# Kernel optimization log

Measured on AMD Instinct MI355X. Metric: run time of the kernel, lower is better.

Reference implementation:

```python
import jax, jax.numpy as jnp
import numpy as np

V = 32000; D = 256; H = 8; L = 2; FF = 1024; S = 512; B = 32
M = 4096          # mem_max_entries
NC = 10           # num_classes
K = 4             # retrieve top-k
TH = 0.5          # write threshold
EPS = 1e-8


def setup_inputs() -> dict:
    key = jax.random.key(0)
    ks = jax.random.split(key, 24)
    s = 0.02
    def nrm(k, shape):
        return jax.random.normal(k, shape, jnp.float32) * s
    return {
        "input_ids": jax.random.randint(ks[0], (B, S), 0, V),
        "tok_emb": nrm(ks[1], (V, D)),
        "pos_emb": nrm(ks[2], (S, D)),
        # per-layer params stacked on leading dim L
        "Wqkv": nrm(ks[3], (L, 3 * D, D)), "bqkv": jnp.zeros((L, 3 * D)),
        "Wo": nrm(ks[4], (L, D, D)), "bo": jnp.zeros((L, D)),
        "ln1_g": jnp.ones((L, D)), "ln1_b": jnp.zeros((L, D)),
        "W1": nrm(ks[5], (L, FF, D)), "b1": jnp.zeros((L, FF)),
        "W2": nrm(ks[6], (L, D, FF)), "b2": jnp.zeros((L, D)),
        "ln2_g": jnp.ones((L, D)), "ln2_b": jnp.zeros((L, D)),
        # write gate MLP (d -> d -> 1, sigmoid)
        "Wg1": nrm(ks[7], (D, D)), "bg1": jnp.zeros((D,)),
        "Wg2": nrm(ks[8], (1, D)), "bg2": jnp.zeros((1,)),
        # classifier
        "Wc": nrm(ks[9], (NC, D)), "bc": jnp.zeros((NC,)),
    }


def _layer_norm(x, g, b):
    m = x.mean(-1, keepdims=True)
    v = ((x - m) ** 2).mean(-1, keepdims=True)
    return (x - m) / jnp.sqrt(v + 1e-5) * g + b


def _encoder_layer(x, Wqkv, bqkv, Wo, bo, g1, b1, W1, bf1, W2, bf2, g2, b2):
    # post-LN TransformerEncoderLayer, relu activation, batch_first
    Bx, Sx, Dx = x.shape
    dh = Dx // H
    qkv = x @ Wqkv.T + bqkv                     # [B,S,3D]
    q, k, v = jnp.split(qkv, 3, axis=-1)
    def heads(t):
        return t.reshape(Bx, Sx, H, dh).transpose(0, 2, 1, 3)  # [B,H,S,dh]
    q, k, v = heads(q), heads(k), heads(v)
    scores = jnp.einsum("bhqd,bhkd->bhqk", q, k) / jnp.sqrt(jnp.float32(dh))
    attn = jax.nn.softmax(scores, axis=-1)
    o = jnp.einsum("bhqk,bhkd->bhqd", attn, v)
    o = o.transpose(0, 2, 1, 3).reshape(Bx, Sx, Dx)
    o = o @ Wo.T + bo
    x = _layer_norm(x + o, g1, b1)
    ff = jax.nn.relu(x @ W1.T + bf1) @ W2.T + bf2
    return _layer_norm(x + ff, g2, b2)


def reference(input_ids, tok_emb, pos_emb, Wqkv, bqkv, Wo, bo, ln1_g, ln1_b,
              W1, b1, W2, b2, ln2_g, ln2_b, Wg1, bg1, Wg2, bg2, Wc, bc):
    Bx, Sx = input_ids.shape
    x = tok_emb[input_ids] + pos_emb[jnp.arange(Sx)][None, :, :]
    for l in range(L):
        x = _encoder_layer(x, Wqkv[l], bqkv[l], Wo[l], bo[l], ln1_g[l], ln1_b[l],
                           W1[l], b1[l], W2[l], b2[l], ln2_g[l], ln2_b[l])
    h = x                                        # [B,S,D]
    cls_state = h[:, 0, :]                       # [B,D]

    # --- write gate: per-token store into external memory (capped FIFO scatter) ---
    flat_h = h.reshape(-1, D)                    # [B*S, D]
    probs = jax.nn.sigmoid(jax.nn.relu(flat_h @ Wg1.T + bg1) @ Wg2.T + bg2)[:, 0]
    mask = probs > TH                            # [B*S]
    slot = jnp.cumsum(mask.astype(jnp.int32)) - 1
    valid = mask & (slot < M)
    idx = jnp.where(valid, slot, M)              # overflow -> dummy row M
    mem = jnp.zeros((M + 1, D), jnp.float32).at[idx].set(flat_h)[:M]
    count = jnp.minimum(mask.sum(), M)
    occupied = jnp.arange(M) < count             # [M]

    # --- top-k cosine retrieval with CLS as query ---
    qn = cls_state / (jnp.linalg.norm(cls_state, axis=-1, keepdims=True) + EPS)
    kn = mem / (jnp.linalg.norm(mem, axis=-1, keepdims=True) + EPS)
    sims = qn @ kn.T                             # [B,M]
    sims = jnp.where(occupied[None, :], sims, -1e9)
    top_sims, top_idx = jax.lax.top_k(sims, K)   # [B,K]
    vals = mem[top_idx]                          # [B,K,D] (unoccupied rows are zero)
    attn = jax.nn.softmax(top_sims, axis=-1)
    mem_vec = jnp.einsum("bk,bkd->bd", attn, vals)
    mem_vec = jnp.where(count > 0, mem_vec, 0.0)

    cls_aug = cls_state + mem_vec
    return cls_aug @ Wc.T + bc                   # [B,NC]
```

## Files before the change

kernel.cpp:

```cpp
#include <hip/hip_runtime.h>
#include <math.h>

#define D_   256
#define H_   8
#define L_   2
#define FF_  1024
#define S_   512
#define B_   32
#define M_   4096
#define NC_  10
#define ROWS (B_*S_)

typedef __attribute__((ext_vector_type(8))) short bf16x8;
typedef __attribute__((ext_vector_type(4))) float f32x4;

__device__ __forceinline__ float wave_sum(float v) {
#pragma unroll
  for (int off = 1; off < 64; off <<= 1) v += __shfl_xor(v, off, 64);
  return v;
}

__device__ __forceinline__ unsigned short bf16_rne(float x) {
  unsigned int b = __float_as_uint(x);
  return (unsigned short)((b + 0x7FFFu + ((b >> 16) & 1u)) >> 16);
}
__device__ __forceinline__ float bf16_f(unsigned short h) {
  return __uint_as_float(((unsigned int)h) << 16);
}
__device__ __forceinline__ unsigned int cvt_pk_bf16(float a, float b) {
  unsigned int r;
  asm volatile("v_cvt_pk_bf16_f32 %0, %1, %2" : "=v"(r) : "v"(a), "v"(b));
  return r;
}

__device__ __forceinline__ void cvt_store(unsigned short* Hq, unsigned short* Lq,
                                          int off, float4 v) {
  float f[4] = {v.x, v.y, v.z, v.w};
  unsigned short h[4], l[4];
#pragma unroll
  for (int i = 0; i < 4; i++) {
    h[i] = bf16_rne(f[i]);
    l[i] = bf16_rne(f[i] - bf16_f(h[i]));
  }
  uint2 hp, lp;
  hp.x = (unsigned int)h[0] | ((unsigned int)h[1] << 16);
  hp.y = (unsigned int)h[2] | ((unsigned int)h[3] << 16);
  lp.x = (unsigned int)l[0] | ((unsigned int)l[1] << 16);
  lp.y = (unsigned int)l[2] | ((unsigned int)l[3] << 16);
  *(uint2*)&Hq[off] = hp;
  *(uint2*)&Lq[off] = lp;
}

__device__ __forceinline__ bf16x8 ld_frag(const unsigned short* p, int off) {
  union { uint2 u[2]; bf16x8 v; } x;
  x.u[0] = *(const uint2*)(p + off);
  x.u[1] = *(const uint2*)(p + off + 4);
  return x.v;
}

__global__ __launch_bounds__(256) void emb_kernel(const int* __restrict__ ids,
                                                  const float* __restrict__ tok,
                                                  const float* __restrict__ pos,
                                                  float* __restrict__ x) {
  const int row  = blockIdx.x * 4 + (threadIdx.x >> 6);
  const int lane = threadIdx.x & 63;
  const int id = ids[row];
  const int s  = row & (S_ - 1);
  const float4 t = *(const float4*)(tok + (size_t)id * D_ + lane * 4);
  const float4 p = *(const float4*)(pos + (size_t)s  * D_ + lane * 4);
  float4 r; r.x = t.x + p.x; r.y = t.y + p.y; r.z = t.z + p.z; r.w = t.w + p.w;
  *(float4*)(x + (size_t)row * D_ + lane * 4) = r;
}

#define LP 36
template<int BM, int RELU>
__global__ __launch_bounds__(512, 4) void gemm_mfma(const float* __restrict__ A,
                                                    const float* __restrict__ Bm,
                                                    const float* __restrict__ bias,
                                                    float* __restrict__ C,
                                                    int M, int N, int K) {
  constexpr int WGM = BM / 64;
  constexpr int WGN = 8 / WGM;
  constexpr int WN  = 128 / WGN;
  constexpr int FN  = WN / 16;
  __shared__ __align__(16) unsigned short Ah[BM * LP];
  __shared__ __align__(16) unsigned short Al[BM * LP];
  __shared__ __align__(16) unsigned short Bh[128 * LP];
  __shared__ __align__(16) unsigned short Bl[128 * LP];

  const int tid  = threadIdx.x;
  const int lane = tid & 63;
  const int wid  = tid >> 6;
  const int wm = wid / WGN, wn = wid % WGN;
  const int m0 = blockIdx.y * BM, n0 = blockIdx.x * 128;
  const int lrow  = lane & 15;
  const int khalf = (lane >> 4) * 8;

  const int srow = tid >> 3;
  const int kq   = (tid & 7) << 2;
  const float* Aptr = A + (size_t)(m0 + srow) * K + kq;
  const float* Bptr = Bm + (size_t)(n0 + srow) * K + kq;

  f32x4 acc[4][FN];
#pragma unroll
  for (int i = 0; i < 4; i++)
#pragma unroll
    for (int j = 0; j < FN; j++) acc[i][j] = (f32x4){0.f, 0.f, 0.f, 0.f};

  float4 pa[BM / 64], pb[2];
#pragma unroll
  for (int j = 0; j < BM / 64; j++) pa[j] = *(const float4*)(Aptr + (size_t)j * 64 * K);
#pragma unroll
  for (int j = 0; j < 2; j++) pb[j] = *(const float4*)(Bptr + (size_t)j * 64 * K);

  for (int k0 = 0; k0 < K; k0 += 32) {
    const int kn = (k0 + 32 < K) ? (k0 + 32) : k0;
    float4 na[BM / 64], nb[2];
#pragma unroll
    for (int j = 0; j < BM / 64; j++) na[j] = *(const float4*)(Aptr + (size_t)j * 64 * K + kn);
#pragma unroll
    for (int j = 0; j < 2; j++) nb[j] = *(const float4*)(Bptr + (size_t)j * 64 * K + kn);

    __syncthreads();
#pragma unroll
    for (int j = 0; j < BM / 64; j++)
      cvt_store(Ah, Al, (srow + j * 64) * LP + kq, pa[j]);
#pragma unroll
    for (int j = 0; j < 2; j++)
      cvt_store(Bh, Bl, (srow + j * 64) * LP + kq, pb[j]);
    __syncthreads();

    bf16x8 ah[4], al[4], bh[FN], bl[FN];
#pragma unroll
    for (int fm = 0; fm < 4; fm++) {
      const int r = (wm * 64 + fm * 16 + lrow) * LP + khalf;
      ah[fm] = ld_frag(Ah, r);
      al[fm] = ld_frag(Al, r);
    }
#pragma unroll
    for (int fn = 0; fn < FN; fn++) {
      const int r = (wn * WN + fn * 16 + lrow) * LP + khalf;
      bh[fn] = ld_frag(Bh, r);
      bl[fn] = ld_frag(Bl, r);
    }
#pragma unroll
    for (int fm = 0; fm < 4; fm++)
#pragma unroll
      for (int fn = 0; fn < FN; fn++) {
        acc[fm][fn] = __builtin_amdgcn_mfma_f32_16x16x32_bf16(ah[fm], bh[fn], acc[fm][fn], 0, 0, 0);
        acc[fm][fn] = __builtin_amdgcn_mfma_f32_16x16x32_bf16(ah[fm], bl[fn], acc[fm][fn], 0, 0, 0);
        acc[fm][fn] = __builtin_amdgcn_mfma_f32_16x16x32_bf16(al[fm], bh[fn], acc[fm][fn], 0, 0, 0);
      }
#pragma unroll
    for (int j = 0; j < BM / 64; j++) pa[j] = na[j];
#pragma unroll
    for (int j = 0; j < 2; j++) pb[j] = nb[j];
  }

#pragma unroll
  for (int fm = 0; fm < 4; fm++)
#pragma unroll
    for (int fn = 0; fn < FN; fn++) {
      const int mrow = m0 + wm * 64 + fm * 16 + (lane >> 4) * 4;
      const int ncol = n0 + wn * WN + fn * 16 + (lane & 15);
      const float bi = bias[ncol];
#pragma unroll
      for (int r = 0; r < 4; r++) {
        float v = acc[fm][fn][r] + bi;
        if (RELU) v = fmaxf(v, 0.f);
        C[(size_t)(mrow + r) * N + ncol] = v;
      }
    }
}

#define KP 36
#define VP 516
__global__ __launch_bounds__(1024, 4) void attn_mfma(const float* __restrict__ qkv,
                                                     float* __restrict__ o) {
  __shared__ __align__(16) unsigned short Kh[512 * KP];
  __shared__ __align__(16) unsigned short Kl[512 * KP];
  __shared__ __align__(16) unsigned short Vth[32 * VP];
  __shared__ __align__(16) unsigned short Vtl[32 * VP];

  const int bh = blockIdx.x;
  const int b = bh >> 3, h = bh & 7;
  const int tid = threadIdx.x;
  const int lane = tid & 63;
  const int wv = tid >> 6;
  const float* base = qkv + (size_t)b * (S_ * 768) + h * 32;

  if (tid < 512) {
    const int slot = tid;
    const int s5 = slot & 31;
    const int orig = (slot & ~31) + 8 * ((s5 >> 2) & 3) + ((s5 >> 4) << 2) + (s5 & 3);
    const float* p = base + (size_t)orig * 768 + 256;
#pragma unroll
    for (int j = 0; j < 8; j++) {
      const float4 v = *(const float4*)(p + j * 4);
      cvt_store(Kh, Kl, slot * KP + j * 4, v);
    }
  } else {
    const int u  = tid - 512;
    const int kp = u & 255;
    const int dg = (u >> 8) * 16;
    const float* p0 = base + (size_t)(2 * kp) * 768 + 512 + dg;
    const float* p1 = p0 + 768;
    float v0[16], v1[16];
#pragma unroll
    for (int i = 0; i < 4; i++) {
      *(float4*)&v0[i * 4] = *(const float4*)(p0 + i * 4);
      *(float4*)&v1[i * 4] = *(const float4*)(p1 + i * 4);
    }
#pragma unroll
    for (int d = 0; d < 16; d++) {
      const unsigned short h0 = bf16_rne(v0[d]), h1 = bf16_rne(v1[d]);
      const unsigned short l0 = bf16_rne(v0[d] - bf16_f(h0));
      const unsigned short l1 = bf16_rne(v1[d] - bf16_f(h1));
      *(unsigned int*)&Vth[(dg + d) * VP + 2 * kp] = (unsigned int)h0 | ((unsigned int)h1 << 16);
      *(unsigned int*)&Vtl[(dg + d) * VP + 2 * kp] = (unsigned int)l0 | ((unsigned int)l1 << 16);
    }
  }

  const int q0 = wv * 32;
  bf16x8 qh[2], ql[2];
#pragma unroll
  for (int f = 0; f < 2; f++) {
    const float* qp = base + (size_t)(q0 + f * 16 + (lane & 15)) * 768 + ((lane >> 4) * 8);
    float qq[8];
    *(float4*)&qq[0] = *(const float4*)qp;
    *(float4*)&qq[4] = *(const float4*)(qp + 4);
    bf16x8 vh, vl;
#pragma unroll
    for (int j = 0; j < 8; j++) {
      const float sv = qq[j] * 0.17677669529663687f;
      const unsigned short hh = bf16_rne(sv);
      vh[j] = (short)hh;
      vl[j] = (short)bf16_rne(sv - bf16_f(hh));
    }
    qh[f] = vh; ql[f] = vl;
  }

  __syncthreads();

  f32x4 oacc[2][2];
#pragma unroll
  for (int i = 0; i < 2; i++)
#pragma unroll
    for (int j = 0; j < 2; j++) oacc[i][j] = (f32x4){0.f, 0.f, 0.f, 0.f};
  float lacc[2] = {0.f, 0.f};

  for (int kt = 0; kt < S_; kt += 32) {
    bf16x8 kah[2], kal[2];
#pragma unroll
    for (int u = 0; u < 2; u++) {
      const int off = (kt + u * 16 + (lane & 15)) * KP + ((lane >> 4) * 8);
      kah[u] = ld_frag(Kh, off);
      kal[u] = ld_frag(Kl, off);
    }
    bf16x8 vah[2], val[2];
#pragma unroll
    for (int df = 0; df < 2; df++) {
      const int off = (df * 16 + (lane & 15)) * VP + kt + ((lane >> 4) * 8);
      vah[df] = ld_frag(Vth, off);
      val[df] = ld_frag(Vtl, off);
    }
    f32x4 s[2][2];
#pragma unroll
    for (int u = 0; u < 2; u++)
#pragma unroll
      for (int f = 0; f < 2; f++) {
        f32x4 a = (f32x4){0.f, 0.f, 0.f, 0.f};
        a = __builtin_amdgcn_mfma_f32_16x16x32_bf16(kal[u], qh[f], a, 0, 0, 0);
        a = __builtin_amdgcn_mfma_f32_16x16x32_bf16(kah[u], ql[f], a, 0, 0, 0);
        a = __builtin_amdgcn_mfma_f32_16x16x32_bf16(kah[u], qh[f], a, 0, 0, 0);
        s[u][f] = a;
      }
#pragma unroll
    for (int f = 0; f < 2; f++) {
      union { unsigned int w[4]; bf16x8 v; } ph, pl;
#pragma unroll
      for (int u = 0; u < 2; u++) {
        const float p0 = __expf(s[u][f][0]);
        const float p1 = __expf(s[u][f][1]);
        const float p2 = __expf(s[u][f][2]);
        const float p3 = __expf(s[u][f][3]);
        lacc[f] += (p0 + p1) + (p2 + p3);
        const unsigned int h01 = cvt_pk_bf16(p0, p1);
        const unsigned int h23 = cvt_pk_bf16(p2, p3);
        const float r0 = p0 - __uint_as_float(h01 << 16);
        const float r1 = p1 - __uint_as_float(h01 & 0xffff0000u);
        const float r2 = p2 - __uint_as_float(h23 << 16);
        const float r3 = p3 - __uint_as_float(h23 & 0xffff0000u);
        ph.w[u * 2 + 0] = h01;
        ph.w[u * 2 + 1] = h23;
        pl.w[u * 2 + 0] = cvt_pk_bf16(r0, r1);
        pl.w[u * 2 + 1] = cvt_pk_bf16(r2, r3);
      }
#pragma unroll
      for (int df = 0; df < 2; df++) {
        oacc[df][f] = __builtin_amdgcn_mfma_f32_16x16x32_bf16(val[df], ph.v, oacc[df][f], 0, 0, 0);
        oacc[df][f] = __builtin_amdgcn_mfma_f32_16x16x32_bf16(vah[df], pl.v, oacc[df][f], 0, 0, 0);
        oacc[df][f] = __builtin_amdgcn_mfma_f32_16x16x32_bf16(vah[df], ph.v, oacc[df][f], 0, 0, 0);
      }
    }
  }

#pragma unroll
  for (int f = 0; f < 2; f++) {
    lacc[f] += __shfl_xor(lacc[f], 16, 64);
    lacc[f] += __shfl_xor(lacc[f], 32, 64);
  }
#pragma unroll
  for (int f = 0; f < 2; f++) {
    const float inv = 1.f / lacc[f];
    const int q = q0 + f * 16 + (lane & 15);
    float* op = o + (size_t)(b * S_ + q) * D_ + h * 32;
#pragma unroll
    for (int df = 0; df < 2; df++) {
      const int dbase = df * 16 + (lane >> 4) * 4;
#pragma unroll
      for (int r = 0; r < 4; r++)
        op[dbase + r] = oacc[df][f][r] * inv;
    }
  }
}

__global__ __launch_bounds__(256) void add_ln(const float* __restrict__ x,
                                              const float* __restrict__ y,
                                              const float* __restrict__ g,
                                              const float* __restrict__ bta,
                                              float* __restrict__ out) {
  const int row  = blockIdx.x * 4 + (threadIdx.x >> 6);
  const int lane = threadIdx.x & 63;
  const size_t base = (size_t)row * D_ + lane * 4;
  const float4 xv = *(const float4*)(x + base);
  const float4 yv = *(const float4*)(y + base);
  float v[4] = {xv.x + yv.x, xv.y + yv.y, xv.z + yv.z, xv.w + yv.w};
  float s = v[0] + v[1] + v[2] + v[3];
  s = wave_sum(s);
  const float mean = s * (1.f / 256.f);
  float d[4] = {v[0] - mean, v[1] - mean, v[2] - mean, v[3] - mean};
  float sq = d[0] * d[0] + d[1] * d[1] + d[2] * d[2] + d[3] * d[3];
  sq = wave_sum(sq);
  const float inv = 1.f / sqrtf(sq * (1.f / 256.f) + 1e-5f);
  const float4 gv = *(const float4*)(g + lane * 4);
  const float4 bv = *(const float4*)(bta + lane * 4);
  float4 r;
  r.x = d[0] * inv * gv.x + bv.x; r.y = d[1] * inv * gv.y + bv.y;
  r.z = d[2] * inv * gv.z + bv.z; r.w = d[3] * inv * gv.w + bv.w;
  *(float4*)(out + base) = r;
}

__global__ __launch_bounds__(256) void gate_mask(const float* __restrict__ t,
                                                 const float* __restrict__ Wg2,
                                                 const float* __restrict__ bg2,
                                                 int* __restrict__ mask) {
  const int row  = blockIdx.x * 4 + (threadIdx.x >> 6);
  const int lane = threadIdx.x & 63;
  const float4 tv = *(const float4*)(t + (size_t)row * D_ + lane * 4);
  const float4 wv = *(const float4*)(Wg2 + lane * 4);
  float s = tv.x * wv.x + tv.y * wv.y + tv.z * wv.z + tv.w * wv.w;
  s = wave_sum(s);
  if (lane == 0) mask[row] = (s + bg2[0]) > 0.f ? 1 : 0;
}

__global__ __launch_bounds__(256) void scan_kernel(const int* __restrict__ mask,
                                                   int* __restrict__ slots,
                                                   int* __restrict__ countp) {
  __shared__ int wtot[4];
  const int tid = threadIdx.x;
  const int lane = tid & 63, wid = tid >> 6;
  const int base = tid * 64;
  int s = 0;
#pragma unroll 8
  for (int i = 0; i < 64; i++) s += mask[base + i];
  int inc = s;
#pragma unroll
  for (int off = 1; off < 64; off <<= 1) {
    const int t = __shfl_up(inc, off, 64);
    if (lane >= off) inc += t;
  }
  if (lane == 63) wtot[wid] = inc;
  __syncthreads();
  int woff = 0;
#pragma unroll
  for (int w = 0; w < 4; w++) woff += (w < wid) ? wtot[w] : 0;
  const int total = wtot[0] + wtot[1] + wtot[2] + wtot[3];
  if (tid == 0) countp[0] = total < M_ ? total : M_;
  int run = woff + inc - s;
  for (int i = 0; i < 64; i++) {
    const int r = base + i;
    const int mk = mask[r];
    slots[r] = (mk && run < M_) ? run : -1;
    run += mk;
  }
}

__global__ __launch_bounds__(256) void scatter_kernel(const float* __restrict__ h,
                                                      const int* __restrict__ slots,
                                                      float* __restrict__ mem) {
  const int row  = blockIdx.x * 4 + (threadIdx.x >> 6);
  const int lane = threadIdx.x & 63;
  const int sl = slots[row];
  if (sl >= 0)
    *(float4*)(mem + (size_t)sl * D_ + lane * 4) =
        *(const float4*)(h + (size_t)row * D_ + lane * 4);
}

__global__ __launch_bounds__(256) void qnorm_kernel(const float* __restrict__ h,
                                                    float* __restrict__ qden) {
  const int b    = blockIdx.x * 4 + (threadIdx.x >> 6);
  const int lane = threadIdx.x & 63;
  const float4 c = *(const float4*)(h + (size_t)b * S_ * D_ + lane * 4);
  float sq = c.x * c.x + c.y * c.y + c.z * c.z + c.w * c.w;
  sq = wave_sum(sq);
  if (lane == 0) qden[b] = sqrtf(sq) + 1e-8f;
}

__global__ __launch_bounds__(256) void sims_kernel(const float* __restrict__ h,
                                                   const float* __restrict__ mem,
                                                   const float* __restrict__ qden,
                                                   const int* __restrict__ countp,
                                                   float* __restrict__ sims) {
  __shared__ float cls[B_ * D_];
  __shared__ float qd[B_];
  const int tid = threadIdx.x;
  const int lane = tid & 63, wid = tid >> 6;
  for (int i = tid; i < B_ * D_ / 4; i += 256) {
    const int flat = i * 4;
    const int b = flat >> 8, d = flat & 255;
    *(float4*)&cls[flat] = *(const float4*)(h + (size_t)b * S_ * D_ + d);
  }
  if (tid < B_) qd[tid] = qden[tid];
  __syncthreads();
  const int count = countp[0];
  const int r = blockIdx.x * 4 + wid;
  const float4 m4 = *(const float4*)(mem + (size_t)r * D_ + lane * 4);
  float sq = m4.x * m4.x + m4.y * m4.y + m4.z * m4.z + m4.w * m4.w;
  sq = wave_sum(sq);
  const float rn = sqrtf(sq) + 1e-8f;
  if (r < count) {
    for (int b = 0; b < B_; b++) {
      const float4 c4 = *(const float4*)&cls[b * D_ + lane * 4];
      float dt = m4.x * c4.x + m4.y * c4.y + m4.z * c4.z + m4.w * c4.w;
      dt = wave_sum(dt);
      if (lane == 0) sims[b * M_ + r] = dt / (qd[b] * rn);
    }
  } else if (lane == 0) {
    for (int b = 0; b < B_; b++) sims[b * M_ + r] = -1e9f;
  }
}

__global__ __launch_bounds__(256) void topk_mix(const float* __restrict__ h,
                                                const float* __restrict__ mem,
                                                const float* __restrict__ simsg,
                                                const int* __restrict__ countp,
                                                const float* __restrict__ Wc,
                                                const float* __restrict__ bc,
                                                float* __restrict__ out) {
  __shared__ float sims[M_];
  __shared__ float cls[D_];
  __shared__ float wv4[4];
  __shared__ int   wi4[4];
  __shared__ float aug[D_];
  __shared__ float tv[4];
  __shared__ int   tix[4];

  const int b = blockIdx.x, tid = threadIdx.x;
  const int lane = tid & 63, wid = tid >> 6;
  const int count = countp[0];

  for (int i = tid; i < M_; i += 256) sims[i] = simsg[b * M_ + i];
  cls[tid] = h[(size_t)b * S_ * D_ + tid];
  __syncthreads();

  for (int k = 0; k < 4; k++) {
    float bv = -INFINITY; int bi = 1 << 30;
#pragma unroll
    for (int rr = 0; rr < M_ / 256; rr++) {
      const int r = tid + rr * 256;
      const float v = sims[r];
      if (v > bv || (v == bv && r < bi)) { bv = v; bi = r; }
    }
#pragma unroll
    for (int off = 1; off < 64; off <<= 1) {
      const float ov = __shfl_xor(bv, off, 64);
      const int   oi = __shfl_xor(bi, off, 64);
      if (ov > bv || (ov == bv && oi < bi)) { bv = ov; bi = oi; }
    }
    if (lane == 0) { wv4[wid] = bv; wi4[wid] = bi; }
    __syncthreads();
    if (tid == 0) {
      float bb = wv4[0]; int bbi = wi4[0];
#pragma unroll
      for (int i = 1; i < 4; i++)
        if (wv4[i] > bb || (wv4[i] == bb && wi4[i] < bbi)) { bb = wv4[i]; bbi = wi4[i]; }
      tv[k] = bb; tix[k] = bbi; sims[bbi] = -INFINITY;
    }
    __syncthreads();
  }

  float w[4];
  {
    const float mx = tv[0];
    float ws = 0.f;
#pragma unroll
    for (int k = 0; k < 4; k++) { w[k] = expf(tv[k] - mx); ws += w[k]; }
    const float inv = 1.f / ws;
#pragma unroll
    for (int k = 0; k < 4; k++) w[k] *= inv;
  }

  {
    float mv = 0.f;
    if (count > 0) {
#pragma unroll
      for (int k = 0; k < 4; k++) mv = fmaf(w[k], mem[(size_t)tix[k] * D_ + tid], mv);
    }
    aug[tid] = cls[tid] + mv;
  }
  __syncthreads();

  const float4 a4 = *(const float4*)&aug[lane * 4];
  for (int c = wid; c < NC_; c += 4) {
    const float4 wc = *(const float4*)(Wc + (size_t)c * D_ + lane * 4);
    float dt = a4.x * wc.x + a4.y * wc.y + a4.z * wc.z + a4.w * wc.w;
    dt = wave_sum(dt);
    if (lane == 0) out[b * NC_ + c] = dt + bc[c];
  }
}

extern "C" void kernel_launch(void* const* d_in, const int* in_sizes, int n_in,
                              void* d_out, int out_size, void* d_ws, size_t ws_size,
                              hipStream_t stream) {
  const int*   ids  = (const int*)d_in[0];
  const float* tok  = (const float*)d_in[1];
  const float* pos  = (const float*)d_in[2];
  const float* Wqkv = (const float*)d_in[3];
  const float* bqkv = (const float*)d_in[4];
  const float* Wo   = (const float*)d_in[5];
  const float* bo   = (const float*)d_in[6];
  const float* ln1g = (const float*)d_in[7];
  const float* ln1b = (const float*)d_in[8];
  const float* W1   = (const float*)d_in[9];
  const float* b1   = (const float*)d_in[10];
  const float* W2   = (const float*)d_in[11];
  const float* b2   = (const float*)d_in[12];
  const float* ln2g = (const float*)d_in[13];
  const float* ln2b = (const float*)d_in[14];
  const float* Wg1  = (const float*)d_in[15];
  const float* bg1  = (const float*)d_in[16];
  const float* Wg2  = (const float*)d_in[17];
  const float* bg2  = (const float*)d_in[18];
  const float* Wc   = (const float*)d_in[19];
  const float* bc   = (const float*)d_in[20];
  float* out = (float*)d_out;

  float* xA   = (float*)d_ws;
  float* xB   = xA  + (size_t)ROWS * D_;
  float* ob   = xB  + (size_t)ROWS * D_;
  float* pb   = ob  + (size_t)ROWS * D_;
  float* big  = pb  + (size_t)ROWS * D_;
  float* mem  = big + (size_t)ROWS * FF_;
  float* qden = mem + (size_t)M_ * D_;
  float* sims = qden + 64;
  int*   mask = (int*)(sims + (size_t)B_ * M_);
  int*   slots = mask + ROWS;
  int*   cnt   = slots + ROWS;

  emb_kernel<<<ROWS / 4, 256, 0, stream>>>(ids, tok, pos, xA);

  for (int l = 0; l < L_; l++) {
    gemm_mfma<128, 0><<<dim3(768 / 128, ROWS / 128), 512, 0, stream>>>(
        xA, Wqkv + (size_t)l * 768 * 256, bqkv + l * 768, big, ROWS, 768, 256);
    attn_mfma<<<B_ * H_, 1024, 0, stream>>>(big, ob);
    gemm_mfma<64, 0><<<dim3(256 / 128, ROWS / 64), 512, 0, stream>>>(
        ob, Wo + (size_t)l * 256 * 256, bo + l * 256, pb, ROWS, 256, 256);
    add_ln<<<ROWS / 4, 256, 0, stream>>>(xA, pb, ln1g + l * 256, ln1b + l * 256, xB);
    gemm_mfma<128, 1><<<dim3(1024 / 128, ROWS / 128), 512, 0, stream>>>(
        xB, W1 + (size_t)l * 1024 * 256, b1 + l * 1024, big, ROWS, 1024, 256);
    gemm_mfma<64, 0><<<dim3(256 / 128, ROWS / 64), 512, 0, stream>>>(
        big, W2 + (size_t)l * 256 * 1024, b2 + l * 256, pb, ROWS, 256, 1024);
    add_ln<<<ROWS / 4, 256, 0, stream>>>(xB, pb, ln2g + l * 256, ln2b + l * 256, xA);
  }

  gemm_mfma<64, 1><<<dim3(256 / 128, ROWS / 64), 512, 0, stream>>>(
      xA, Wg1, bg1, ob, ROWS, 256, 256);
  gate_mask<<<ROWS / 4, 256, 0, stream>>>(ob, Wg2, bg2, mask);
  scan_kernel<<<1, 256, 0, stream>>>(mask, slots, cnt);
  (void)hipMemsetAsync(mem, 0, (size_t)M_ * D_ * sizeof(float), stream);
  scatter_kernel<<<ROWS / 4, 256, 0, stream>>>(xA, slots, mem);

  qnorm_kernel<<<B_ / 4, 256, 0, stream>>>(xA, qden);
  sims_kernel<<<M_ / 4, 256, 0, stream>>>(xA, mem, qden, cnt, sims);
  topk_mix<<<B_, 256, 0, stream>>>(xA, mem, sims, cnt, Wc, bc, out);
}
```

Measured before the change: 471.9 us.

## Store activations and weights as packed bf16 hi/lo pairs to skip per-tile conversion

Producers (embedding, layernorm, GEMM epilogues, attention output) now write each value as a packed 32-bit hi/lo bf16 split, and weights are packed once per call by a new kernel. GEMM and attention loads then only unpack bits into LDS instead of redoing the split conversion on every tile load. GEMM and attention grids are flattened with a block-index swizzle across groups of eight, likely for XCD/L2 locality. This adds extra packed buffers and duplicate writes in add_ln and emb, plus five weight-packing launches on every call.

```diff
diff --git a/kernel.cpp b/kernel.cpp
--- a/kernel.cpp
+++ b/kernel.cpp
@@ -13,6 +13,8 @@
 
 typedef __attribute__((ext_vector_type(8))) short bf16x8;
 typedef __attribute__((ext_vector_type(4))) float f32x4;
+typedef unsigned int uint32;
+typedef unsigned short ushort16;
 
 __device__ __forceinline__ float wave_sum(float v) {
 #pragma unroll
@@ -27,30 +29,21 @@
 __device__ __forceinline__ float bf16_f(unsigned short h) {
   return __uint_as_float(((unsigned int)h) << 16);
 }
-__device__ __forceinline__ unsigned int cvt_pk_bf16(float a, float b) {
-  unsigned int r;
-  asm volatile("v_cvt_pk_bf16_f32 %0, %1, %2" : "=v"(r) : "v"(a), "v"(b));
-  return r;
-}
-
-__device__ __forceinline__ void cvt_store(unsigned short* Hq, unsigned short* Lq,
-                                          int off, float4 v) {
-  float f[4] = {v.x, v.y, v.z, v.w};
-  unsigned short h[4], l[4];
-#pragma unroll
-  for (int i = 0; i < 4; i++) {
-    h[i] = bf16_rne(f[i]);
-    l[i] = bf16_rne(f[i] - bf16_f(h[i]));
-  }
+__device__ __forceinline__ uint32 pack_split(float x) {
+  const unsigned short h = bf16_rne(x);
+  const unsigned short l = bf16_rne(x - bf16_f(h));
+  return (uint32)h | ((uint32)l << 16);
+}
+__device__ __forceinline__ void unpack_store(unsigned short* Hq, unsigned short* Lq,
+                                             int off, uint4 v) {
   uint2 hp, lp;
-  hp.x = (unsigned int)h[0] | ((unsigned int)h[1] << 16);
-  hp.y = (unsigned int)h[2] | ((unsigned int)h[3] << 16);
-  lp.x = (unsigned int)l[0] | ((unsigned int)l[1] << 16);
-  lp.y = (unsigned int)l[2] | ((unsigned int)l[3] << 16);
+  hp.x = (v.x & 0xffffu) | (v.y << 16);
+  hp.y = (v.z & 0xffffu) | (v.w << 16);
+  lp.x = (v.x >> 16) | (v.y & 0xffff0000u);
+  lp.y = (v.z >> 16) | (v.w & 0xffff0000u);
   *(uint2*)&Hq[off] = hp;
   *(uint2*)&Lq[off] = lp;
 }
-
 __device__ __forceinline__ bf16x8 ld_frag(const unsigned short* p, int off) {
   union { uint2 u[2]; bf16x8 v; } x;
   x.u[0] = *(const uint2*)(p + off);
@@ -58,10 +51,23 @@
   return x.v;
 }
 
+__global__ __launch_bounds__(256) void pack_f32(const float* __restrict__ src,
+                                                uint32* __restrict__ dst, int n4) {
+  const int i = blockIdx.x * 256 + threadIdx.x;
+  if (i < n4) {
+    const float4 v = ((const float4*)src)[i];
+    uint4 o;
+    o.x = pack_split(v.x); o.y = pack_split(v.y);
+    o.z = pack_split(v.z); o.w = pack_split(v.w);
+    ((uint4*)dst)[i] = o;
+  }
+}
+
 __global__ __launch_bounds__(256) void emb_kernel(const int* __restrict__ ids,
                                                   const float* __restrict__ tok,
                                                   const float* __restrict__ pos,
-                                                  float* __restrict__ x) {
+                                                  float* __restrict__ x,
+                                                  uint32* __restrict__ xp) {
   const int row  = blockIdx.x * 4 + (threadIdx.x >> 6);
   const int lane = threadIdx.x & 63;
   const int id = ids[row];
@@ -70,15 +76,20 @@
   const float4 p = *(const float4*)(pos + (size_t)s  * D_ + lane * 4);
   float4 r; r.x = t.x + p.x; r.y = t.y + p.y; r.z = t.z + p.z; r.w = t.w + p.w;
   *(float4*)(x + (size_t)row * D_ + lane * 4) = r;
+  uint4 o;
+  o.x = pack_split(r.x); o.y = pack_split(r.y);
+  o.z = pack_split(r.z); o.w = pack_split(r.w);
+  *(uint4*)(xp + (size_t)row * D_ + lane * 4) = o;
 }
 
 #define LP 36
-template<int BM, int RELU>
-__global__ __launch_bounds__(512, 4) void gemm_mfma(const float* __restrict__ A,
-                                                    const float* __restrict__ Bm,
+template<int BM, int RELU, int PACKOUT>
+__global__ __launch_bounds__(512, 4) void gemm_mfma(const uint32* __restrict__ Ap,
+                                                    const uint32* __restrict__ Bp,
                                                     const float* __restrict__ bias,
                                                     float* __restrict__ C,
-                                                    int M, int N, int K) {
+                                                    uint32* __restrict__ Cp,
+                                                    int M, int N, int K, int NX) {
   constexpr int WGM = BM / 64;
   constexpr int WGN = 8 / WGM;
   constexpr int WN  = 128 / WGN;
@@ -88,18 +99,22 @@
   __shared__ __align__(16) unsigned short Bh[128 * LP];
   __shared__ __align__(16) unsigned short Bl[128 * LP];
 
+  const int q8 = gridDim.x >> 3;
+  const int orig = (blockIdx.x & 7) * q8 + (blockIdx.x >> 3);
+  const int by = orig / NX, bx = orig % NX;
+
   const int tid  = threadIdx.x;
   const int lane = tid & 63;
   const int wid  = tid >> 6;
   const int wm = wid / WGN, wn = wid % WGN;
-  const int m0 = blockIdx.y * BM, n0 = blockIdx.x * 128;
+  const int m0 = by * BM, n0 = bx * 128;
   const int lrow  = lane & 15;
   const int khalf = (lane >> 4) * 8;
 
   const int srow = tid >> 3;
   const int kq   = (tid & 7) << 2;
-  const float* Aptr = A + (size_t)(m0 + srow) * K + kq;
-  const float* Bptr = Bm + (size_t)(n0 + srow) * K + kq;
+  const uint32* Aptr = Ap + (size_t)(m0 + srow) * K + kq;
+  const uint32* Bptr = Bp + (size_t)(n0 + srow) * K + kq;
 
   f32x4 acc[4][FN];
 #pragma unroll
@@ -107,27 +122,27 @@
 #pragma unroll
     for (int j = 0; j < FN; j++) acc[i][j] = (f32x4){0.f, 0.f, 0.f, 0.f};
 
-  float4 pa[BM / 64], pb[2];
-#pragma unroll
-  for (int j = 0; j < BM / 64; j++) pa[j] = *(const float4*)(Aptr + (size_t)j * 64 * K);
-#pragma unroll
-  for (int j = 0; j < 2; j++) pb[j] = *(const float4*)(Bptr + (size_t)j * 64 * K);
+  uint4 pa[BM / 64], pb[2];
+#pragma unroll
+  for (int j = 0; j < BM / 64; j++) pa[j] = *(const uint4*)(Aptr + (size_t)j * 64 * K);
+#pragma unroll
+  for (int j = 0; j < 2; j++) pb[j] = *(const uint4*)(Bptr + (size_t)j * 64 * K);
 
   for (int k0 = 0; k0 < K; k0 += 32) {
     const int kn = (k0 + 32 < K) ? (k0 + 32) : k0;
-    float4 na[BM / 64], nb[2];
-#pragma unroll
-    for (int j = 0; j < BM / 64; j++) na[j] = *(const float4*)(Aptr + (size_t)j * 64 * K + kn);
-#pragma unroll
-    for (int j = 0; j < 2; j++) nb[j] = *(const float4*)(Bptr + (size_t)j * 64 * K + kn);
+    uint4 na[BM / 64], nb[2];
+#pragma unroll
+    for (int j = 0; j < BM / 64; j++) na[j] = *(const uint4*)(Aptr + (size_t)j * 64 * K + kn);
+#pragma unroll
+    for (int j = 0; j < 2; j++) nb[j] = *(const uint4*)(Bptr + (size_t)j * 64 * K + kn);
 
     __syncthreads();
 #pragma unroll
     for (int j = 0; j < BM / 64; j++)
-      cvt_store(Ah, Al, (srow + j * 64) * LP + kq, pa[j]);
+      unpack_store(Ah, Al, (srow + j * 64) * LP + kq, pa[j]);
 #pragma unroll
     for (int j = 0; j < 2; j++)
-      cvt_store(Bh, Bl, (srow + j * 64) * LP + kq, pb[j]);
+      unpack_store(Bh, Bl, (srow + j * 64) * LP + kq, pb[j]);
     __syncthreads();
 
     bf16x8 ah[4], al[4], bh[FN], bl[FN];
@@ -168,56 +183,54 @@
       for (int r = 0; r < 4; r++) {
         float v = acc[fm][fn][r] + bi;
         if (RELU) v = fmaxf(v, 0.f);
-        C[(size_t)(mrow + r) * N + ncol] = v;
+        if (PACKOUT) Cp[(size_t)(mrow + r) * N + ncol] = pack_split(v);
+        else         C[(size_t)(mrow + r) * N + ncol] = v;
       }
     }
 }
 
 #define KP 36
 #define VP 516
-__global__ __launch_bounds__(1024, 4) void attn_mfma(const float* __restrict__ qkv,
-                                                     float* __restrict__ o) {
+__global__ __launch_bounds__(1024, 4) void attn_mfma(const uint32* __restrict__ qkv,
+                                                     uint32* __restrict__ o) {
   __shared__ __align__(16) unsigned short Kh[512 * KP];
   __shared__ __align__(16) unsigned short Kl[512 * KP];
   __shared__ __align__(16) unsigned short Vth[32 * VP];
   __shared__ __align__(16) unsigned short Vtl[32 * VP];
 
-  const int bh = blockIdx.x;
-  const int b = bh >> 3, h = bh & 7;
+  const int q8g = gridDim.x >> 3;
+  const int obh = (blockIdx.x & 7) * q8g + (blockIdx.x >> 3);
+  const int b = obh >> 3, h = obh & 7;
   const int tid = threadIdx.x;
   const int lane = tid & 63;
   const int wv = tid >> 6;
-  const float* base = qkv + (size_t)b * (S_ * 768) + h * 32;
+  const uint32* base = qkv + (size_t)b * (S_ * 768) + h * 32;
 
   if (tid < 512) {
     const int slot = tid;
     const int s5 = slot & 31;
     const int orig = (slot & ~31) + 8 * ((s5 >> 2) & 3) + ((s5 >> 4) << 2) + (s5 & 3);
-    const float* p = base + (size_t)orig * 768 + 256;
-#pragma unroll
-    for (int j = 0; j < 8; j++) {
-      const float4 v = *(const float4*)(p + j * 4);
-      cvt_store(Kh, Kl, slot * KP + j * 4, v);
-    }
+    const uint32* p = base + (size_t)orig * 768 + 256;
+#pragma unroll
+    for (int j = 0; j < 8; j++)
+      unpack_store(Kh, Kl, slot * KP + j * 4, *(const uint4*)(p + j * 4));
   } else {
     const int u  = tid - 512;
     const int kp = u & 255;
     const int dg = (u >> 8) * 16;
-    const float* p0 = base + (size_t)(2 * kp) * 768 + 512 + dg;
-    const float* p1 = p0 + 768;
-    float v0[16], v1[16];
+    const uint32* p0 = base + (size_t)(2 * kp) * 768 + 512 + dg;
+    const uint32* p1 = p0 + 768;
+    union { uint4 u4[4]; uint32 w[16]; } a0, a1;
 #pragma unroll
     for (int i = 0; i < 4; i++) {
-      *(float4*)&v0[i * 4] = *(const float4*)(p0 + i * 4);
-      *(float4*)&v1[i * 4] = *(const float4*)(p1 + i * 4);
+      a0.u4[i] = *(const uint4*)(p0 + i * 4);
+      a1.u4[i] = *(const uint4*)(p1 + i * 4);
     }
 #pragma unroll
     for (int d = 0; d < 16; d++) {
-      const unsigned short h0 = bf16_rne(v0[d]), h1 = bf16_rne(v1[d]);
-      const unsigned short l0 = bf16_rne(v0[d] - bf16_f(h0));
-      const unsigned short l1 = bf16_rne(v1[d] - bf16_f(h1));
-      *(unsigned int*)&Vth[(dg + d) * VP + 2 * kp] = (unsigned int)h0 | ((unsigned int)h1 << 16);
-      *(unsigned int*)&Vtl[(dg + d) * VP + 2 * kp] = (unsigned int)l0 | ((unsigned int)l1 << 16);
+      const uint32 w0 = a0.w[d], w1 = a1.w[d];
+      *(uint32*)&Vth[(dg + d) * VP + 2 * kp] = (w0 & 0xffffu) | (w1 << 16);
+      *(uint32*)&Vtl[(dg + d) * VP + 2 * kp] = (w0 >> 16) | (w1 & 0xffff0000u);
     }
   }
 
@@ -225,14 +238,16 @@
   bf16x8 qh[2], ql[2];
 #pragma unroll
   for (int f = 0; f < 2; f++) {
-    const float* qp = base + (size_t)(q0 + f * 16 + (lane & 15)) * 768 + ((lane >> 4) * 8);
-    float qq[8];
-    *(float4*)&qq[0] = *(const float4*)qp;
-    *(float4*)&qq[4] = *(const float4*)(qp + 4);
+    const uint32* qp = base + (size_t)(q0 + f * 16 + (lane & 15)) * 768 + ((lane >> 4) * 8);
+    union { uint4 u4[2]; uint32 w[8]; } qu;
+    qu.u4[0] = *(const uint4*)qp;
+    qu.u4[1] = *(const uint4*)(qp + 4);
     bf16x8 vh, vl;
 #pragma unroll
     for (int j = 0; j < 8; j++) {
-      const float sv = qq[j] * 0.17677669529663687f;
+      const uint32 p = qu.w[j];
+      const float qf = __uint_as_float(p << 16) + __uint_as_float(p & 0xffff0000u);
+      const float sv = qf * 0.17677669529663687f;
       const unsigned short hh = bf16_rne(sv);
       vh[j] = (short)hh;
       vl[j] = (short)bf16_rne(sv - bf16_f(hh));
@@ -277,7 +292,7 @@
       }
 #pragma unroll
     for (int f = 0; f < 2; f++) {
-      union { unsigned int w[4]; bf16x8 v; } ph, pl;
+      union { uint32 w[4]; bf16x8 v; } ph, pl;
 #pragma unroll
       for (int u = 0; u < 2; u++) {
         const float p0 = __expf(s[u][f][0]);
@@ -285,16 +300,20 @@
         const float p2 = __expf(s[u][f][2]);
         const float p3 = __expf(s[u][f][3]);
         lacc[f] += (p0 + p1) + (p2 + p3);
-        const unsigned int h01 = cvt_pk_bf16(p0, p1);
-        const unsigned int h23 = cvt_pk_bf16(p2, p3);
+        unsigned int h01, h23;
+        asm volatile("v_cvt_pk_bf16_f32 %0, %1, %2" : "=v"(h01) : "v"(p0), "v"(p1));
+        asm volatile("v_cvt_pk_bf16_f32 %0, %1, %2" : "=v"(h23) : "v"(p2), "v"(p3));
         const float r0 = p0 - __uint_as_float(h01 << 16);
         const float r1 = p1 - __uint_as_float(h01 & 0xffff0000u);
         const float r2 = p2 - __uint_as_float(h23 << 16);
         const float r3 = p3 - __uint_as_float(h23 & 0xffff0000u);
+        unsigned int l01, l23;
+        asm volatile("v_cvt_pk_bf16_f32 %0, %1, %2" : "=v"(l01) : "v"(r0), "v"(r1));
+        asm volatile("v_cvt_pk_bf16_f32 %0, %1, %2" : "=v"(l23) : "v"(r2), "v"(r3));
         ph.w[u * 2 + 0] = h01;
         ph.w[u * 2 + 1] = h23;
-        pl.w[u * 2 + 0] = cvt_pk_bf16(r0, r1);
-        pl.w[u * 2 + 1] = cvt_pk_bf16(r2, r3);
+        pl.w[u * 2 + 0] = l01;
+        pl.w[u * 2 + 1] = l23;
       }
 #pragma unroll
       for (int df = 0; df < 2; df++) {
@@ -314,13 +333,13 @@
   for (int f = 0; f < 2; f++) {
     const float inv = 1.f / lacc[f];
     const int q = q0 + f * 16 + (lane & 15);
-    float* op = o + (size_t)(b * S_ + q) * D_ + h * 32;
+    uint32* op = o + (size_t)(b * S_ + q) * D_ + h * 32;
 #pragma unroll
     for (int df = 0; df < 2; df++) {
       const int dbase = df * 16 + (lane >> 4) * 4;
 #pragma unroll
       for (int r = 0; r < 4; r++)
-        op[dbase + r] = oacc[df][f][r] * inv;
+        op[dbase + r] = pack_split(oacc[df][f][r] * inv);
     }
   }
 }
@@ -329,7 +348,8 @@
                                               const float* __restrict__ y,
                                               const float* __restrict__ g,
                                               const float* __restrict__ bta,
-                                              float* __restrict__ out) {
+                                              float* __restrict__ out,
+                                              uint32* __restrict__ outp) {
   const int row  = blockIdx.x * 4 + (threadIdx.x >> 6);
   const int lane = threadIdx.x & 63;
   const size_t base = (size_t)row * D_ + lane * 4;
@@ -349,6 +369,10 @@
   r.x = d[0] * inv * gv.x + bv.x; r.y = d[1] * inv * gv.y + bv.y;
   r.z = d[2] * inv * gv.z + bv.z; r.w = d[3] * inv * gv.w + bv.w;
   *(float4*)(out + base) = r;
+  uint4 o;
+  o.x = pack_split(r.x); o.y = pack_split(r.y);
+  o.z = pack_split(r.z); o.w = pack_split(r.w);
+  *(uint4*)(outp + base) = o;
 }
 
 __global__ __launch_bounds__(256) void gate_mask(const float* __restrict__ t,
@@ -556,37 +580,50 @@
   const float* bc   = (const float*)d_in[20];
   float* out = (float*)d_out;
 
-  float* xA   = (float*)d_ws;
-  float* xB   = xA  + (size_t)ROWS * D_;
-  float* ob   = xB  + (size_t)ROWS * D_;
-  float* pb   = ob  + (size_t)ROWS * D_;
-  float* big  = pb  + (size_t)ROWS * D_;
-  float* mem  = big + (size_t)ROWS * FF_;
-  float* qden = mem + (size_t)M_ * D_;
-  float* sims = qden + 64;
-  int*   mask = (int*)(sims + (size_t)B_ * M_);
-  int*   slots = mask + ROWS;
-  int*   cnt   = slots + ROWS;
-
-  emb_kernel<<<ROWS / 4, 256, 0, stream>>>(ids, tok, pos, xA);
+  float*  xA    = (float*)d_ws;
+  float*  xB    = xA  + (size_t)ROWS * D_;
+  float*  pb    = xB  + (size_t)ROWS * D_;
+  uint32* xAp   = (uint32*)(pb + (size_t)ROWS * D_);
+  uint32* xBp   = xAp + (size_t)ROWS * D_;
+  uint32* obp   = xBp + (size_t)ROWS * D_;
+  uint32* bigp  = obp + (size_t)ROWS * D_;
+  uint32* Wqkvp = bigp + (size_t)ROWS * FF_;
+  uint32* Wop   = Wqkvp + (size_t)L_ * 768 * 256;
+  uint32* W1p   = Wop   + (size_t)L_ * 256 * 256;
+  uint32* W2p   = W1p   + (size_t)L_ * 1024 * 256;
+  uint32* Wg1p  = W2p   + (size_t)L_ * 256 * 1024;
+  float*  mem   = (float*)(Wg1p + 256 * 256);
+  float*  qden  = mem + (size_t)M_ * D_;
+  float*  sims  = qden + 64;
+  int*    mask  = (int*)(sims + (size_t)B_ * M_);
+  int*    slots = mask + ROWS;
+  int*    cnt   = slots + ROWS;
+
+  pack_f32<<<(L_ * 768 * 256 / 4 + 255) / 256, 256, 0, stream>>>(Wqkv, Wqkvp, L_ * 768 * 256 / 4);
+  pack_f32<<<(L_ * 256 * 256 / 4 + 255) / 256, 256, 0, stream>>>(Wo, Wop, L_ * 256 * 256 / 4);
+  pack_f32<<<(L_ * 1024 * 256 / 4 + 255) / 256, 256, 0, stream>>>(W1, W1p, L_ * 1024 * 256 / 4);
+  pack_f32<<<(L_ * 256 * 1024 / 4 + 255) / 256, 256, 0, stream>>>(W2, W2p, L_ * 256 * 1024 / 4);
+  pack_f32<<<(256 * 256 / 4 + 255) / 256, 256, 0, stream>>>(Wg1, Wg1p, 256 * 256 / 4);
+
+  emb_kernel<<<ROWS / 4, 256, 0, stream>>>(ids, tok, pos, xA, xAp);
 
   for (int l = 0; l < L_; l++) {
-    gemm_mfma<128, 0><<<dim3(768 / 128, ROWS / 128), 512, 0, stream>>>(
-        xA, Wqkv + (size_t)l * 768 * 256, bqkv + l * 768, big, ROWS, 768, 256);
-    attn_mfma<<<B_ * H_, 1024, 0, stream>>>(big, ob);
-    gemm_mfma<64, 0><<<dim3(256 / 128, ROWS / 64), 512, 0, stream>>>(
-        ob, Wo + (size_t)l * 256 * 256, bo + l * 256, pb, ROWS, 256, 256);
-    add_ln<<<ROWS / 4, 256, 0, stream>>>(xA, pb, ln1g + l * 256, ln1b + l * 256, xB);
-    gemm_mfma<128, 1><<<dim3(1024 / 128, ROWS / 128), 512, 0, stream>>>(
-        xB, W1 + (size_t)l * 1024 * 256, b1 + l * 1024, big, ROWS, 1024, 256);
-    gemm_mfma<64, 0><<<dim3(256 / 128, ROWS / 64), 512, 0, stream>>>(
-        big, W2 + (size_t)l * 256 * 1024, b2 + l * 256, pb, ROWS, 256, 1024);
-    add_ln<<<ROWS / 4, 256, 0, stream>>>(xB, pb, ln2g + l * 256, ln2b + l * 256, xA);
-  }
-
-  gemm_mfma<64, 1><<<dim3(256 / 128, ROWS / 64), 512, 0, stream>>>(
-      xA, Wg1, bg1, ob, ROWS, 256, 256);
-  gate_mask<<<ROWS / 4, 256, 0, stream>>>(ob, Wg2, bg2, mask);
+    gemm_mfma<128, 0, 1><<<768, 512, 0, stream>>>(
+        xAp, Wqkvp + (size_t)l * 768 * 256, bqkv + l * 768, nullptr, bigp, ROWS, 768, 256, 6);
+    attn_mfma<<<B_ * H_, 1024, 0, stream>>>(bigp, obp);
+    gemm_mfma<64, 0, 0><<<512, 512, 0, stream>>>(
+        obp, Wop + (size_t)l * 256 * 256, bo + l * 256, pb, nullptr, ROWS, 256, 256, 2);
+    add_ln<<<ROWS / 4, 256, 0, stream>>>(xA, pb, ln1g + l * 256, ln1b + l * 256, xB, xBp);
+    gemm_mfma<128, 1, 1><<<1024, 512, 0, stream>>>(
+        xBp, W1p + (size_t)l * 1024 * 256, b1 + l * 1024, nullptr, bigp, ROWS, 1024, 256, 8);
+    gemm_mfma<64, 0, 0><<<512, 512, 0, stream>>>(
+        bigp, W2p + (size_t)l * 256 * 1024, b2 + l * 256, pb, nullptr, ROWS, 256, 1024, 2);
+    add_ln<<<ROWS / 4, 256, 0, stream>>>(xB, pb, ln2g + l * 256, ln2b + l * 256, xA, xAp);
+  }
+
+  gemm_mfma<64, 1, 0><<<512, 512, 0, stream>>>(
+      xAp, Wg1p, bg1, pb, nullptr, ROWS, 256, 256, 2);
+  gate_mask<<<ROWS / 4, 256, 0, stream>>>(pb, Wg2, bg2, mask);
   scan_kernel<<<1, 256, 0, stream>>>(mask, slots, cnt);
   (void)hipMemsetAsync(mem, 0, (size_t)M_ * D_ * sizeof(float), stream);
   scatter_kernel<<<ROWS / 4, 256, 0, stream>>>(xA, slots, mem);
```

Result: faster. 455.4 us (-3.5%).
